# Optimization experiments

Hardware: AMD Instinct MI355X
Metric: run time of the kernel (lower is better)

Reference implementation:

```python
import jax, jax.numpy as jnp
import numpy as np

DIM = 512
HEADS = 8
BLOCKS = 6
DFF = 2048
B = 4
T = 2048
VOCAB = 20
CLASSES = 1
MAX_TOKENS = 5000
EPS = 1e-5


def _make_pe():
    # Sinusoidal positional encoding, identical to PositionalEncodingSin
    pos = np.arange(MAX_TOKENS, dtype=np.float32)[:, None]
    div = np.exp(np.arange(0, DIM, 2, dtype=np.float32) * (-np.log(10000.0) / DIM))
    pe = np.zeros((MAX_TOKENS, DIM), dtype=np.float32)
    pe[:, 0::2] = np.sin(pos * div)
    pe[:, 1::2] = np.cos(pos * div)
    return jnp.asarray(pe)


def setup_inputs() -> dict:
    key = jax.random.key(0)
    ks = jax.random.split(key, 8)

    def n(k, shape, s=0.02):
        return (jax.random.normal(k, shape) * s).astype(jnp.float32)

    x = jax.random.randint(ks[0], (B, T), 0, VOCAB, dtype=jnp.int32)
    embed = n(ks[1], (VOCAB, DIM))
    pe = _make_pe()
    Wqkv = n(ks[2], (BLOCKS, DIM, 3 * DIM))   # to_qvk (no bias)
    W0 = n(ks[3], (BLOCKS, DIM, DIM))          # W_0 (no bias)
    g1 = jnp.ones((BLOCKS, DIM), jnp.float32)
    b1 = jnp.zeros((BLOCKS, DIM), jnp.float32)
    g2 = jnp.ones((BLOCKS, DIM), jnp.float32)
    b2 = jnp.zeros((BLOCKS, DIM), jnp.float32)
    Wl1 = n(ks[4], (BLOCKS, DIM, DFF))
    bl1 = jnp.zeros((BLOCKS, DFF), jnp.float32)
    Wl2 = n(ks[5], (BLOCKS, DFF, DIM))
    bl2 = jnp.zeros((BLOCKS, DIM), jnp.float32)
    Whead = n(ks[6], (DIM, CLASSES))
    bhead = jnp.zeros((CLASSES,), jnp.float32)
    return dict(x=x, embed=embed, pe=pe, Wqkv=Wqkv, W0=W0, g1=g1, b1=b1,
                g2=g2, b2=b2, Wl1=Wl1, bl1=bl1, Wl2=Wl2, bl2=bl2,
                Whead=Whead, bhead=bhead)


def _ln(x, g, b):
    mu = x.mean(-1, keepdims=True)
    var = ((x - mu) ** 2).mean(-1, keepdims=True)
    return (x - mu) / jnp.sqrt(var + EPS) * g + b


def _mhsa(x, Wqkv, W0):
    b, t, _ = x.shape
    dh = DIM // HEADS
    qkv = x @ Wqkv                                   # [b, t, 3*DIM]
    # rearrange 'b t (d k h) -> k b h t d' with k=3, h=HEADS
    qkv = qkv.reshape(b, t, dh, 3, HEADS).transpose(3, 0, 4, 1, 2)
    q, k, v = qkv[0], qkv[1], qkv[2]                 # [b, h, t, dh]
    scores = jnp.einsum('bhid,bhjd->bhij', q, k) * (dh ** -0.5)
    attn = jax.nn.softmax(scores, axis=-1)
    out = jnp.einsum('bhij,bhjd->bhid', attn, v)
    out = out.transpose(0, 2, 1, 3).reshape(b, t, DIM)  # 'b h t d -> b t (h d)'
    return out @ W0


def _forward(x, embed, pe, Wqkv, W0, g1, b1, g2, b2, Wl1, bl1, Wl2, bl2, Whead, bhead):
    h = embed[x] + pe[None, :x.shape[1], :]          # embedding + sinusoidal PE (dropout off)
    for i in range(BLOCKS):                          # post-norm transformer blocks
        a = _mhsa(h, Wqkv[i], W0[i])
        y = _ln(a + h, g1[i], b1[i])
        m = jax.nn.gelu(y @ Wl1[i] + bl1[i], approximate=False) @ Wl2[i] + bl2[i]
        h = _ln(m + y, g2[i], b2[i])
    return (h @ Whead + bhead).squeeze(-1)           # [B, T]


def reference(x, embed, pe, Wqkv, W0, g1, b1, g2, b2, Wl1, bl1, Wl2, bl2, Whead, bhead):
    return _forward(x, embed, pe, Wqkv, W0, g1, b1, g2, b2, Wl1, bl1, Wl2, bl2, Whead, bhead)
```

## Files before the change

kernel.cpp:

```cpp
#include <hip/hip_runtime.h>
#include <hip/hip_bf16.h>
#include <math.h>

#define DIMD 512
#define HEADS 8
#define NBLK 6
#define DFF 2048
#define BATCH 4
#define SEQ 2048
#define NTOK 8192
#define DH 64
#define LNEPS 1e-5f
#define QSCALE 0.1803368801111204f

typedef __bf16 bf16;
typedef __bf16 bf16x8 __attribute__((ext_vector_type(8)));
typedef __bf16 bf16x4 __attribute__((ext_vector_type(4)));
typedef float f32x4 __attribute__((ext_vector_type(4)));
typedef float f32x16 __attribute__((ext_vector_type(16)));

__device__ __forceinline__ void async16(const void* g, void* l) {
  __builtin_amdgcn_global_load_lds(
      (const __attribute__((address_space(1))) void*)g,
      (__attribute__((address_space(3))) void*)l, 16, 0, 0);
}

__device__ __forceinline__ int swz(int r) { return ((r >> 1) ^ (r >> 3)) & 3; }

__global__ void k_cvt_t(const float* __restrict__ in, bf16* __restrict__ out, int K, int N) {
  __shared__ float T[32][33];
  const float* src = in + (size_t)blockIdx.z * K * N;
  bf16* dst = out + (size_t)blockIdx.z * K * N;
  int k0 = blockIdx.y * 32, n0 = blockIdx.x * 32;
  int r = threadIdx.x >> 3, c4 = (threadIdx.x & 7) * 4;
  float4 v = *reinterpret_cast<const float4*>(src + (size_t)(k0 + r) * N + n0 + c4);
  T[r][c4] = v.x; T[r][c4 + 1] = v.y; T[r][c4 + 2] = v.z; T[r][c4 + 3] = v.w;
  __syncthreads();
  bf16x4 o;
  o[0] = (bf16)T[c4][r]; o[1] = (bf16)T[c4 + 1][r];
  o[2] = (bf16)T[c4 + 2][r]; o[3] = (bf16)T[c4 + 3][r];
  *reinterpret_cast<bf16x4*>(dst + (size_t)(n0 + r) * K + k0 + c4) = o;
}

__global__ void k_cvt_qkv(const float* __restrict__ in, bf16* __restrict__ out, int K, int N) {
  __shared__ float T[32][33];
  const float* src = in + (size_t)blockIdx.z * K * N;
  bf16* dst = out + (size_t)blockIdx.z * K * N;
  int k0 = blockIdx.y * 32, n0 = blockIdx.x * 32;
  int r = threadIdx.x >> 3, c4 = (threadIdx.x & 7) * 4;
  float4 v = *reinterpret_cast<const float4*>(src + (size_t)(k0 + r) * N + n0 + c4);
  T[r][c4] = v.x; T[r][c4 + 1] = v.y; T[r][c4 + 2] = v.z; T[r][c4 + 3] = v.w;
  __syncthreads();
  int n_src = n0 + r;
  int d = n_src / 24;
  int rem = n_src - d * 24;
  int np = (rem >> 3) * 512 + (rem & 7) * 64 + d;
  bf16x4 o;
  o[0] = (bf16)T[c4][r]; o[1] = (bf16)T[c4 + 1][r];
  o[2] = (bf16)T[c4 + 2][r]; o[3] = (bf16)T[c4 + 3][r];
  *reinterpret_cast<bf16x4*>(dst + (size_t)np * K + k0 + c4) = o;
}

__global__ void k_embed(const int* __restrict__ x, const float* __restrict__ embed,
                        const float* __restrict__ pe, bf16* __restrict__ hb,
                        float* __restrict__ hf) {
  int row = blockIdx.x;
  int t = row & (SEQ - 1);
  int tok = x[row];
  int c = threadIdx.x * 2;
  const float* e = embed + (size_t)tok * DIMD;
  const float* p = pe + (size_t)t * DIMD;
  float v0 = e[c] + p[c];
  float v1 = e[c + 1] + p[c + 1];
  size_t o = (size_t)row * DIMD + c;
  hb[o] = (bf16)v0; hb[o + 1] = (bf16)v1;
  hf[o] = v0;       hf[o + 1] = v1;
}

enum { EPI_QKV = 0, EPI_RES = 1, EPI_GELU = 2, EPI_BIASRES = 3 };

template <int EPI, int MT>
__global__ __launch_bounds__(256) void k_gemm(
    const bf16* __restrict__ A, const bf16* __restrict__ Wt,
    const float* __restrict__ bias, const float* __restrict__ resf,
    bf16* __restrict__ out0, bf16* __restrict__ out1, bf16* __restrict__ out2,
    float* __restrict__ outf, int N, int K) {
  constexpr int TJ = (MT == 128) ? 2 : 1;
  __shared__ bf16 As[2][MT][32];
  __shared__ bf16 Bs[2][128][32];
  int tid = threadIdx.x;
  int w = tid >> 6, lane = tid & 63, hi = lane >> 5, l31 = lane & 31;
  int m0 = blockIdx.y * MT, n0 = blockIdx.x * 128;
  int wr = (MT == 128) ? (w >> 1) : 0;
  int wc = (MT == 128) ? (w & 1) : w;

  const bf16 *Ag0, *Ag1 = nullptr, *Bg0, *Bg1;
  int dA0, dA1 = 0, dB0, dB1;
  if (MT == 128) {
    int ra0 = w * 32 + (lane >> 2), ra1 = ra0 + 16;
    Ag0 = A + (size_t)(m0 + ra0) * K + ((lane & 3) ^ swz(ra0)) * 8;
    Ag1 = A + (size_t)(m0 + ra1) * K + ((lane & 3) ^ swz(ra1)) * 8;
    Bg0 = Wt + (size_t)(n0 + ra0) * K + ((lane & 3) ^ swz(ra0)) * 8;
    Bg1 = Wt + (size_t)(n0 + ra1) * K + ((lane & 3) ^ swz(ra1)) * 8;
    dA0 = w * 1024; dA1 = dA0 + 512;
    dB0 = w * 1024; dB1 = dB0 + 512;
  } else {
    int ra = w * 16 + (lane >> 2);
    Ag0 = A + (size_t)(m0 + ra) * K + ((lane & 3) ^ swz(ra)) * 8;
    int rb1 = ra + 64;
    Bg0 = Wt + (size_t)(n0 + ra) * K + ((lane & 3) ^ swz(ra)) * 8;
    Bg1 = Wt + (size_t)(n0 + rb1) * K + ((lane & 3) ^ swz(rb1)) * 8;
    dA0 = w * 512;
    dB0 = w * 512; dB1 = dB0 + 2048;
  }

  int rowA[2], fA[2], colB[2], fB[2];
#pragma unroll
  for (int i = 0; i < 2; ++i) {
    rowA[i] = ((MT == 128) ? wr * 64 : 0) + i * 32 + l31;
    fA[i] = swz(rowA[i]);
  }
#pragma unroll
  for (int j = 0; j < TJ; ++j) {
    colB[j] = ((MT == 128) ? (wc * 64 + j * 32) : (wc * 32)) + l31;
    fB[j] = swz(colB[j]);
  }

  f32x16 acc[2][TJ] = {};

  auto stage = [&](int it) {
    int buf = it & 1;
    bf16* a = &As[buf][0][0];
    bf16* b = &Bs[buf][0][0];
    int k0 = it * 32;
    async16(Ag0 + k0, a + dA0);
    if (MT == 128) async16(Ag1 + k0, a + dA1);
    async16(Bg0 + k0, b + dB0);
    async16(Bg1 + k0, b + dB1);
  };

  int nit = K / 32;
  stage(0);
  for (int it = 0; it < nit; ++it) {
    int buf = it & 1;
    __syncthreads();
    if (it + 1 < nit) stage(it + 1);
#pragma unroll
    for (int s = 0; s < 2; ++s) {
      int lc = s * 2 + hi;
      bf16x8 af[2], bfr[TJ];
#pragma unroll
      for (int i = 0; i < 2; ++i)
        af[i] = *reinterpret_cast<const bf16x8*>(&As[buf][rowA[i]][(lc ^ fA[i]) * 8]);
#pragma unroll
      for (int j = 0; j < TJ; ++j)
        bfr[j] = *reinterpret_cast<const bf16x8*>(&Bs[buf][colB[j]][(lc ^ fB[j]) * 8]);
#pragma unroll
      for (int i = 0; i < 2; ++i)
#pragma unroll
        for (int j = 0; j < TJ; ++j)
          acc[i][j] = __builtin_amdgcn_mfma_f32_32x32x16_bf16(af[i], bfr[j], acc[i][j], 0, 0, 0);
    }
  }

#pragma unroll
  for (int j = 0; j < TJ; ++j) {
    int col = n0 + ((MT == 128) ? (wc * 64 + j * 32) : (wc * 32)) + l31;
    int qwhich = 0, qhh = 0, qdd = 0;
    float bcol = 0.f;
    if (EPI == EPI_QKV) {
      qwhich = col >> 9; qhh = (col >> 6) & 7; qdd = col & 63;
    } else if (EPI == EPI_GELU || EPI == EPI_BIASRES) {
      bcol = bias[col];
    }
#pragma unroll
    for (int i = 0; i < 2; ++i) {
#pragma unroll
      for (int reg = 0; reg < 16; ++reg) {
        int row = m0 + ((MT == 128) ? wr * 64 : 0) + i * 32 + (reg & 3) + 8 * (reg >> 2) + 4 * hi;
        float v = acc[i][j][reg];
        if (EPI == EPI_QKV) {
          int b = row >> 11;
          int t = row & (SEQ - 1);
          int bh = b * HEADS + qhh;
          if (qwhich == 0)      out0[((size_t)bh * SEQ + t) * DH + qdd] = (bf16)(v * QSCALE);
          else if (qwhich == 1) out1[((size_t)bh * SEQ + t) * DH + qdd] = (bf16)v;
          else                  out2[((size_t)bh * DH + qdd) * SEQ + t] = (bf16)v;
        } else if (EPI == EPI_RES) {
          outf[(size_t)row * N + col] = v + resf[(size_t)row * N + col];
        } else if (EPI == EPI_GELU) {
          float xv = v + bcol;
          out0[(size_t)row * N + col] = (bf16)(0.5f * xv * (1.0f + erff(xv * 0.70710678118f)));
        } else {
          outf[(size_t)row * N + col] = v + bcol + resf[(size_t)row * N + col];
        }
      }
    }
  }
}

__global__ __launch_bounds__(256) void k_attn(const bf16* __restrict__ q,
                                              const bf16* __restrict__ k,
                                              const bf16* __restrict__ vt,
                                              bf16* __restrict__ out) {
  __shared__ bf16 Ks[64][64];
  __shared__ bf16 Vs[64][64];
  __shared__ bf16 Pw[4][2][16][72];
  int tid = threadIdx.x;
  int w = tid >> 6, lane = tid & 63, quad = lane >> 4, l15 = lane & 15;
  int f = blockIdx.y * gridDim.x + blockIdx.x;
  int xcd = f & 7, g = f >> 3;
  int bh = xcd * 4 + (g >> 4);
  int qt = g & 15;
  const bf16* qbase = q + (size_t)bh * SEQ * DH;
  const bf16* kbase = k + (size_t)bh * SEQ * DH;
  const bf16* vbase = vt + (size_t)bh * DH * SEQ;

  bf16x8 qf[2][2];
#pragma unroll
  for (int s = 0; s < 2; ++s) {
    int qrow = qt * 128 + s * 64 + w * 16 + l15;
    qf[s][0] = *reinterpret_cast<const bf16x8*>(qbase + (size_t)qrow * DH + quad * 8);
    qf[s][1] = *reinterpret_cast<const bf16x8*>(qbase + (size_t)qrow * DH + 32 + quad * 8);
  }

  int strow = w * 16 + (lane >> 3);
  int scol = ((lane & 7) ^ (lane >> 3)) * 8;
  const bf16* kp = kbase + (size_t)strow * DH + scol;
  const bf16* vp = vbase + (size_t)strow * SEQ + scol;
  bf16* kdst = &Ks[0][0] + (size_t)w * 1024 + (size_t)lane * 8;
  bf16* vdst = &Vs[0][0] + (size_t)w * 1024 + (size_t)lane * 8;

  f32x4 Ot[2][4] = {};
  float ls[2] = {0.f, 0.f};
  int fx = (l15 & 7);

  bf16x8 ka0 = *reinterpret_cast<const bf16x8*>(kp);
  bf16x8 kb0 = *reinterpret_cast<const bf16x8*>(kp + (size_t)8 * DH);
  bf16x8 va0 = *reinterpret_cast<const bf16x8*>(vp);
  bf16x8 vb0 = *reinterpret_cast<const bf16x8*>(vp + (size_t)8 * SEQ);
  bf16x8 ka1 = *reinterpret_cast<const bf16x8*>(kp + (size_t)64 * DH);
  bf16x8 kb1 = *reinterpret_cast<const bf16x8*>(kp + (size_t)72 * DH);
  bf16x8 va1 = *reinterpret_cast<const bf16x8*>(vp + 64);
  bf16x8 vb1 = *reinterpret_cast<const bf16x8*>(vp + 64 + (size_t)8 * SEQ);

  const int nit = SEQ / 64;
  auto body = [&](int it, bf16x8& ka, bf16x8& kb, bf16x8& va, bf16x8& vb) {
    __syncthreads();
    *reinterpret_cast<bf16x8*>(kdst) = ka;
    *reinterpret_cast<bf16x8*>(kdst + 512) = kb;
    *reinterpret_cast<bf16x8*>(vdst) = va;
    *reinterpret_cast<bf16x8*>(vdst + 512) = vb;
    __syncthreads();
    if (it + 2 < nit) {
      size_t ko = (size_t)(it + 2) * 64;
      ka = *reinterpret_cast<const bf16x8*>(kp + ko * DH);
      kb = *reinterpret_cast<const bf16x8*>(kp + ko * DH + 8 * DH);
      va = *reinterpret_cast<const bf16x8*>(vp + ko);
      vb = *reinterpret_cast<const bf16x8*>(vp + ko + (size_t)8 * SEQ);
    }

    f32x4 st[2][4];
#pragma unroll
    for (int nt = 0; nt < 4; ++nt) {
      bf16x8 kf0 = *reinterpret_cast<const bf16x8*>(&Ks[nt * 16 + l15][(quad ^ fx) * 8]);
      bf16x8 kf1 = *reinterpret_cast<const bf16x8*>(&Ks[nt * 16 + l15][((quad + 4) ^ fx) * 8]);
#pragma unroll
      for (int s = 0; s < 2; ++s) {
        f32x4 z = {};
        z = __builtin_amdgcn_mfma_f32_16x16x32_bf16(kf0, qf[s][0], z, 0, 0, 0);
        z = __builtin_amdgcn_mfma_f32_16x16x32_bf16(kf1, qf[s][1], z, 0, 0, 0);
        st[s][nt] = z;
      }
    }

#pragma unroll
    for (int s = 0; s < 2; ++s)
#pragma unroll
      for (int nt = 0; nt < 4; ++nt) {
#pragma unroll
        for (int r = 0; r < 4; ++r) {
          float p = exp2f(st[s][nt][r]);
          st[s][nt][r] = p;
          ls[s] += p;
        }
        bf16x4 pv;
        pv[0] = (bf16)st[s][nt][0]; pv[1] = (bf16)st[s][nt][1];
        pv[2] = (bf16)st[s][nt][2]; pv[3] = (bf16)st[s][nt][3];
        *reinterpret_cast<bf16x4*>(&Pw[w][s][l15][nt * 16 + quad * 4]) = pv;
      }

#pragma unroll
    for (int h = 0; h < 2; ++h) {
      bf16x8 pf0 = *reinterpret_cast<const bf16x8*>(&Pw[w][0][l15][h * 32 + quad * 8]);
      bf16x8 pf1 = *reinterpret_cast<const bf16x8*>(&Pw[w][1][l15][h * 32 + quad * 8]);
#pragma unroll
      for (int nt = 0; nt < 4; ++nt) {
        bf16x8 vf = *reinterpret_cast<const bf16x8*>(&Vs[nt * 16 + l15][((quad + 4 * h) ^ fx) * 8]);
        Ot[0][nt] = __builtin_amdgcn_mfma_f32_16x16x32_bf16(vf, pf0, Ot[0][nt], 0, 0, 0);
        Ot[1][nt] = __builtin_amdgcn_mfma_f32_16x16x32_bf16(vf, pf1, Ot[1][nt], 0, 0, 0);
      }
    }
  };

  for (int it = 0; it < nit; it += 2) {
    body(it, ka0, kb0, va0, vb0);
    body(it + 1, ka1, kb1, va1, vb1);
  }

  int b = bh >> 3, hh = bh & 7;
  int qr = lane >> 2, c0 = (lane & 3) * 16;
#pragma unroll
  for (int s = 0; s < 2; ++s) {
    float l = ls[s];
    l += __shfl_xor(l, 16);
    l += __shfl_xor(l, 32);
    float inv = 1.0f / l;
#pragma unroll
    for (int nt = 0; nt < 4; ++nt) {
      bf16x4 ov;
      ov[0] = (bf16)(Ot[s][nt][0] * inv); ov[1] = (bf16)(Ot[s][nt][1] * inv);
      ov[2] = (bf16)(Ot[s][nt][2] * inv); ov[3] = (bf16)(Ot[s][nt][3] * inv);
      *reinterpret_cast<bf16x4*>(&Pw[w][s][l15][nt * 16 + quad * 4]) = ov;
    }
    bf16x8 o0 = *reinterpret_cast<const bf16x8*>(&Pw[w][s][qr][c0]);
    bf16x8 o1 = *reinterpret_cast<const bf16x8*>(&Pw[w][s][qr][c0 + 8]);
    int token = b * SEQ + qt * 128 + s * 64 + w * 16 + qr;
    *reinterpret_cast<bf16x8*>(out + (size_t)token * DIMD + hh * DH + c0) = o0;
    *reinterpret_cast<bf16x8*>(out + (size_t)token * DIMD + hh * DH + c0 + 8) = o1;
  }
}

__global__ void k_ln(const float* __restrict__ in, const float* __restrict__ g,
                     const float* __restrict__ b, bf16* __restrict__ outb,
                     float* __restrict__ outf) {
  int wid = (blockIdx.x * blockDim.x + threadIdx.x) >> 6;
  int lane = threadIdx.x & 63;
  const float* row = in + (size_t)wid * DIMD;
  float4 x0 = *reinterpret_cast<const float4*>(row + lane * 8);
  float4 x1 = *reinterpret_cast<const float4*>(row + lane * 8 + 4);
  float xs[8] = {x0.x, x0.y, x0.z, x0.w, x1.x, x1.y, x1.z, x1.w};
  float s = 0.f, sq = 0.f;
#pragma unroll
  for (int j = 0; j < 8; ++j) { s += xs[j]; sq += xs[j] * xs[j]; }
#pragma unroll
  for (int m = 1; m < 64; m <<= 1) { s += __shfl_xor(s, m); sq += __shfl_xor(sq, m); }
  float mu = s * (1.0f / DIMD);
  float var = sq * (1.0f / DIMD) - mu * mu;
  float rstd = rsqrtf(var + LNEPS);
  bf16x8 ov;
#pragma unroll
  for (int j = 0; j < 8; ++j) {
    int c = lane * 8 + j;
    float y = (xs[j] - mu) * rstd * g[c] + b[c];
    ov[j] = (bf16)y;
    outf[(size_t)wid * DIMD + c] = y;
  }
  *reinterpret_cast<bf16x8*>(outb + (size_t)wid * DIMD + lane * 8) = ov;
}

__global__ void k_head(const bf16* __restrict__ h, const float* __restrict__ w,
                       const float* __restrict__ bh, float* __restrict__ out) {
  int row = (blockIdx.x * blockDim.x + threadIdx.x) >> 6;
  int lane = threadIdx.x & 63;
  bf16x8 xv = *reinterpret_cast<const bf16x8*>(h + (size_t)row * DIMD + lane * 8);
  float s = 0.f;
#pragma unroll
  for (int j = 0; j < 8; ++j) s += (float)xv[j] * w[lane * 8 + j];
#pragma unroll
  for (int m = 1; m < 64; m <<= 1) s += __shfl_xor(s, m);
  if (lane == 0) out[row] = s + bh[0];
}

extern "C" void kernel_launch(void* const* d_in, const int* in_sizes, int n_in,
                              void* d_out, int out_size, void* d_ws, size_t ws_size,
                              hipStream_t stream) {
  const int*   x     = (const int*)d_in[0];
  const float* embed = (const float*)d_in[1];
  const float* pe    = (const float*)d_in[2];
  const float* Wqkv  = (const float*)d_in[3];
  const float* W0    = (const float*)d_in[4];
  const float* g1    = (const float*)d_in[5];
  const float* b1    = (const float*)d_in[6];
  const float* g2    = (const float*)d_in[7];
  const float* b2    = (const float*)d_in[8];
  const float* Wl1   = (const float*)d_in[9];
  const float* bl1   = (const float*)d_in[10];
  const float* Wl2   = (const float*)d_in[11];
  const float* bl2   = (const float*)d_in[12];
  const float* Whead = (const float*)d_in[13];
  const float* bhead = (const float*)d_in[14];
  float* outp = (float*)d_out;

  char* ws = (char*)d_ws;
  size_t off = 0;
  auto alloc = [&](size_t bytes) { void* p = ws + off; off += (bytes + 255) & ~(size_t)255; return p; };
  const size_t ACT = (size_t)NTOK * DIMD;
  bf16*  hb   = (bf16*)alloc(ACT * 2);
  float* hf   = (float*)alloc(ACT * 4);
  bf16*  qb   = (bf16*)alloc(ACT * 2);
  bf16*  kb   = (bf16*)alloc(ACT * 2);
  bf16*  vtb  = (bf16*)alloc(ACT * 2);
  bf16*  ao   = (bf16*)alloc(ACT * 2);
  float* r32  = (float*)alloc(ACT * 4);
  bf16*  yb   = (bf16*)alloc(ACT * 2);
  float* yf   = (float*)alloc(ACT * 4);
  bf16*  wqkt = (bf16*)alloc((size_t)NBLK * DIMD * 3 * DIMD * 2);
  bf16*  w0t  = (bf16*)alloc((size_t)NBLK * DIMD * DIMD * 2);
  bf16*  wl1t = (bf16*)alloc((size_t)NBLK * DIMD * DFF * 2);
  bf16*  wl2t = (bf16*)alloc((size_t)NBLK * DFF * DIMD * 2);
  bf16*  mid  = qb;

  k_cvt_qkv<<<dim3(3 * DIMD / 32, DIMD / 32, NBLK), 256, 0, stream>>>(Wqkv, wqkt, DIMD, 3 * DIMD);
  k_cvt_t<<<dim3(DIMD / 32, DIMD / 32, NBLK), 256, 0, stream>>>(W0, w0t, DIMD, DIMD);
  k_cvt_t<<<dim3(DFF / 32, DIMD / 32, NBLK), 256, 0, stream>>>(Wl1, wl1t, DIMD, DFF);
  k_cvt_t<<<dim3(DIMD / 32, DFF / 32, NBLK), 256, 0, stream>>>(Wl2, wl2t, DFF, DIMD);

  k_embed<<<NTOK, 256, 0, stream>>>(x, embed, pe, hb, hf);
  for (int i = 0; i < NBLK; ++i) {
    k_gemm<EPI_QKV, 128><<<dim3(3 * DIMD / 128, NTOK / 128), 256, 0, stream>>>(
        hb, wqkt + (size_t)i * DIMD * 3 * DIMD, nullptr, nullptr,
        qb, kb, vtb, nullptr, 3 * DIMD, DIMD);
    k_attn<<<dim3(SEQ / 128, BATCH * HEADS), 256, 0, stream>>>(qb, kb, vtb, ao);
    k_gemm<EPI_RES, 64><<<dim3(DIMD / 128, NTOK / 64), 256, 0, stream>>>(
        ao, w0t + (size_t)i * DIMD * DIMD, nullptr, hf,
        nullptr, nullptr, nullptr, r32, DIMD, DIMD);
    k_ln<<<NTOK / 4, 256, 0, stream>>>(r32, g1 + i * DIMD, b1 + i * DIMD, yb, yf);
    k_gemm<EPI_GELU, 128><<<dim3(DFF / 128, NTOK / 128), 256, 0, stream>>>(
        yb, wl1t + (size_t)i * DIMD * DFF, bl1 + (size_t)i * DFF, nullptr,
        mid, nullptr, nullptr, nullptr, DFF, DIMD);
    k_gemm<EPI_BIASRES, 64><<<dim3(DIMD / 128, NTOK / 64), 256, 0, stream>>>(
        mid, wl2t + (size_t)i * DFF * DIMD, bl2 + (size_t)i * DIMD, yf,
        nullptr, nullptr, nullptr, r32, DIMD, DFF);
    k_ln<<<NTOK / 4, 256, 0, stream>>>(r32, g2 + i * DIMD, b2 + i * DIMD, hb, hf);
  }
  k_head<<<NTOK / 4, 256, 0, stream>>>(hb, Whead, bhead, outp);
}
```

Before: 1.443 ms.

## Keep residual stream in bf16 and drop GEMM LDS double buffering

The fp32 residual and pre-LayerNorm buffers are removed. GEMM epilogues now read a bf16 residual and write a bf16 pre-norm sum, and LayerNorm reads bf16 and writes only bf16, which roughly halves residual traffic and removes the extra fp32 writes. The GEMM main loop also changes from a double-buffered async-load pipeline to a single buffer with loads followed by two barriers per k-step. That gives up load/compute overlap for less LDS, and carrying the residual in bf16 lowers numerical accuracy across six blocks.

```diff
diff --git a/kernel.cpp b/kernel.cpp
--- a/kernel.cpp
+++ b/kernel.cpp
@@ -62,19 +62,16 @@
 }
 
 __global__ void k_embed(const int* __restrict__ x, const float* __restrict__ embed,
-                        const float* __restrict__ pe, bf16* __restrict__ hb,
-                        float* __restrict__ hf) {
+                        const float* __restrict__ pe, bf16* __restrict__ hb) {
   int row = blockIdx.x;
   int t = row & (SEQ - 1);
   int tok = x[row];
   int c = threadIdx.x * 2;
   const float* e = embed + (size_t)tok * DIMD;
   const float* p = pe + (size_t)t * DIMD;
-  float v0 = e[c] + p[c];
-  float v1 = e[c + 1] + p[c + 1];
   size_t o = (size_t)row * DIMD + c;
-  hb[o] = (bf16)v0; hb[o + 1] = (bf16)v1;
-  hf[o] = v0;       hf[o + 1] = v1;
+  hb[o] = (bf16)(e[c] + p[c]);
+  hb[o + 1] = (bf16)(e[c + 1] + p[c + 1]);
 }
 
 enum { EPI_QKV = 0, EPI_RES = 1, EPI_GELU = 2, EPI_BIASRES = 3 };
@@ -82,12 +79,12 @@
 template <int EPI, int MT>
 __global__ __launch_bounds__(256) void k_gemm(
     const bf16* __restrict__ A, const bf16* __restrict__ Wt,
-    const float* __restrict__ bias, const float* __restrict__ resf,
+    const float* __restrict__ bias, const bf16* __restrict__ resb,
     bf16* __restrict__ out0, bf16* __restrict__ out1, bf16* __restrict__ out2,
-    float* __restrict__ outf, int N, int K) {
+    int N, int K) {
   constexpr int TJ = (MT == 128) ? 2 : 1;
-  __shared__ bf16 As[2][MT][32];
-  __shared__ bf16 Bs[2][128][32];
+  __shared__ bf16 As[MT][32];
+  __shared__ bf16 Bs[128][32];
   int tid = threadIdx.x;
   int w = tid >> 6, lane = tid & 63, hi = lane >> 5, l31 = lane & 31;
   int m0 = blockIdx.y * MT, n0 = blockIdx.x * 128;
@@ -95,23 +92,23 @@
   int wc = (MT == 128) ? (w & 1) : w;
 
   const bf16 *Ag0, *Ag1 = nullptr, *Bg0, *Bg1;
-  int dA0, dA1 = 0, dB0, dB1;
+  bf16 *dA0, *dA1 = nullptr, *dB0, *dB1;
   if (MT == 128) {
     int ra0 = w * 32 + (lane >> 2), ra1 = ra0 + 16;
     Ag0 = A + (size_t)(m0 + ra0) * K + ((lane & 3) ^ swz(ra0)) * 8;
     Ag1 = A + (size_t)(m0 + ra1) * K + ((lane & 3) ^ swz(ra1)) * 8;
     Bg0 = Wt + (size_t)(n0 + ra0) * K + ((lane & 3) ^ swz(ra0)) * 8;
     Bg1 = Wt + (size_t)(n0 + ra1) * K + ((lane & 3) ^ swz(ra1)) * 8;
-    dA0 = w * 1024; dA1 = dA0 + 512;
-    dB0 = w * 1024; dB1 = dB0 + 512;
+    dA0 = &As[0][0] + w * 1024; dA1 = dA0 + 512;
+    dB0 = &Bs[0][0] + w * 1024; dB1 = dB0 + 512;
   } else {
     int ra = w * 16 + (lane >> 2);
     Ag0 = A + (size_t)(m0 + ra) * K + ((lane & 3) ^ swz(ra)) * 8;
     int rb1 = ra + 64;
     Bg0 = Wt + (size_t)(n0 + ra) * K + ((lane & 3) ^ swz(ra)) * 8;
     Bg1 = Wt + (size_t)(n0 + rb1) * K + ((lane & 3) ^ swz(rb1)) * 8;
-    dA0 = w * 512;
-    dB0 = w * 512; dB1 = dB0 + 2048;
+    dA0 = &As[0][0] + w * 512;
+    dB0 = &Bs[0][0] + w * 512; dB1 = dB0 + 2048;
   }
 
   int rowA[2], fA[2], colB[2], fB[2];
@@ -128,39 +125,30 @@
 
   f32x16 acc[2][TJ] = {};
 
-  auto stage = [&](int it) {
-    int buf = it & 1;
-    bf16* a = &As[buf][0][0];
-    bf16* b = &Bs[buf][0][0];
-    int k0 = it * 32;
-    async16(Ag0 + k0, a + dA0);
-    if (MT == 128) async16(Ag1 + k0, a + dA1);
-    async16(Bg0 + k0, b + dB0);
-    async16(Bg1 + k0, b + dB1);
-  };
-
-  int nit = K / 32;
-  stage(0);
-  for (int it = 0; it < nit; ++it) {
-    int buf = it & 1;
+  for (int k0 = 0; k0 < K; k0 += 32) {
+    async16(Ag0 + k0, dA0);
+    if (MT == 128) async16(Ag1 + k0, dA1);
+    async16(Bg0 + k0, dB0);
+    async16(Bg1 + k0, dB1);
     __syncthreads();
-    if (it + 1 < nit) stage(it + 1);
+
 #pragma unroll
     for (int s = 0; s < 2; ++s) {
       int lc = s * 2 + hi;
       bf16x8 af[2], bfr[TJ];
 #pragma unroll
       for (int i = 0; i < 2; ++i)
-        af[i] = *reinterpret_cast<const bf16x8*>(&As[buf][rowA[i]][(lc ^ fA[i]) * 8]);
+        af[i] = *reinterpret_cast<const bf16x8*>(&As[rowA[i]][(lc ^ fA[i]) * 8]);
 #pragma unroll
       for (int j = 0; j < TJ; ++j)
-        bfr[j] = *reinterpret_cast<const bf16x8*>(&Bs[buf][colB[j]][(lc ^ fB[j]) * 8]);
+        bfr[j] = *reinterpret_cast<const bf16x8*>(&Bs[colB[j]][(lc ^ fB[j]) * 8]);
 #pragma unroll
       for (int i = 0; i < 2; ++i)
 #pragma unroll
         for (int j = 0; j < TJ; ++j)
           acc[i][j] = __builtin_amdgcn_mfma_f32_32x32x16_bf16(af[i], bfr[j], acc[i][j], 0, 0, 0);
     }
+    __syncthreads();
   }
 
 #pragma unroll
@@ -187,12 +175,12 @@
           else if (qwhich == 1) out1[((size_t)bh * SEQ + t) * DH + qdd] = (bf16)v;
           else                  out2[((size_t)bh * DH + qdd) * SEQ + t] = (bf16)v;
         } else if (EPI == EPI_RES) {
-          outf[(size_t)row * N + col] = v + resf[(size_t)row * N + col];
+          out0[(size_t)row * N + col] = (bf16)(v + (float)resb[(size_t)row * N + col]);
         } else if (EPI == EPI_GELU) {
           float xv = v + bcol;
           out0[(size_t)row * N + col] = (bf16)(0.5f * xv * (1.0f + erff(xv * 0.70710678118f)));
         } else {
-          outf[(size_t)row * N + col] = v + bcol + resf[(size_t)row * N + col];
+          out0[(size_t)row * N + col] = (bf16)(v + bcol + (float)resb[(size_t)row * N + col]);
         }
       }
     }
@@ -331,18 +319,15 @@
   }
 }
 
-__global__ void k_ln(const float* __restrict__ in, const float* __restrict__ g,
-                     const float* __restrict__ b, bf16* __restrict__ outb,
-                     float* __restrict__ outf) {
+__global__ void k_ln(const bf16* __restrict__ in, const float* __restrict__ g,
+                     const float* __restrict__ b, bf16* __restrict__ outb) {
   int wid = (blockIdx.x * blockDim.x + threadIdx.x) >> 6;
   int lane = threadIdx.x & 63;
-  const float* row = in + (size_t)wid * DIMD;
-  float4 x0 = *reinterpret_cast<const float4*>(row + lane * 8);
-  float4 x1 = *reinterpret_cast<const float4*>(row + lane * 8 + 4);
-  float xs[8] = {x0.x, x0.y, x0.z, x0.w, x1.x, x1.y, x1.z, x1.w};
+  bf16x8 xv = *reinterpret_cast<const bf16x8*>(in + (size_t)wid * DIMD + lane * 8);
+  float xs[8];
   float s = 0.f, sq = 0.f;
 #pragma unroll
-  for (int j = 0; j < 8; ++j) { s += xs[j]; sq += xs[j] * xs[j]; }
+  for (int j = 0; j < 8; ++j) { xs[j] = (float)xv[j]; s += xs[j]; sq += xs[j] * xs[j]; }
 #pragma unroll
   for (int m = 1; m < 64; m <<= 1) { s += __shfl_xor(s, m); sq += __shfl_xor(sq, m); }
   float mu = s * (1.0f / DIMD);
@@ -352,9 +337,7 @@
 #pragma unroll
   for (int j = 0; j < 8; ++j) {
     int c = lane * 8 + j;
-    float y = (xs[j] - mu) * rstd * g[c] + b[c];
-    ov[j] = (bf16)y;
-    outf[(size_t)wid * DIMD + c] = y;
+    ov[j] = (bf16)((xs[j] - mu) * rstd * g[c] + b[c]);
   }
   *reinterpret_cast<bf16x8*>(outb + (size_t)wid * DIMD + lane * 8) = ov;
 }
@@ -397,14 +380,12 @@
   auto alloc = [&](size_t bytes) { void* p = ws + off; off += (bytes + 255) & ~(size_t)255; return p; };
   const size_t ACT = (size_t)NTOK * DIMD;
   bf16*  hb   = (bf16*)alloc(ACT * 2);
-  float* hf   = (float*)alloc(ACT * 4);
   bf16*  qb   = (bf16*)alloc(ACT * 2);
   bf16*  kb   = (bf16*)alloc(ACT * 2);
   bf16*  vtb  = (bf16*)alloc(ACT * 2);
   bf16*  ao   = (bf16*)alloc(ACT * 2);
-  float* r32  = (float*)alloc(ACT * 4);
+  bf16*  rb   = (bf16*)alloc(ACT * 2);
   bf16*  yb   = (bf16*)alloc(ACT * 2);
-  float* yf   = (float*)alloc(ACT * 4);
   bf16*  wqkt = (bf16*)alloc((size_t)NBLK * DIMD * 3 * DIMD * 2);
   bf16*  w0t  = (bf16*)alloc((size_t)NBLK * DIMD * DIMD * 2);
   bf16*  wl1t = (bf16*)alloc((size_t)NBLK * DIMD * DFF * 2);
@@ -416,23 +397,23 @@
   k_cvt_t<<<dim3(DFF / 32, DIMD / 32, NBLK), 256, 0, stream>>>(Wl1, wl1t, DIMD, DFF);
   k_cvt_t<<<dim3(DIMD / 32, DFF / 32, NBLK), 256, 0, stream>>>(Wl2, wl2t, DFF, DIMD);
 
-  k_embed<<<NTOK, 256, 0, stream>>>(x, embed, pe, hb, hf);
+  k_embed<<<NTOK, 256, 0, stream>>>(x, embed, pe, hb);
   for (int i = 0; i < NBLK; ++i) {
     k_gemm<EPI_QKV, 128><<<dim3(3 * DIMD / 128, NTOK / 128), 256, 0, stream>>>(
         hb, wqkt + (size_t)i * DIMD * 3 * DIMD, nullptr, nullptr,
-        qb, kb, vtb, nullptr, 3 * DIMD, DIMD);
+        qb, kb, vtb, 3 * DIMD, DIMD);
     k_attn<<<dim3(SEQ / 128, BATCH * HEADS), 256, 0, stream>>>(qb, kb, vtb, ao);
     k_gemm<EPI_RES, 64><<<dim3(DIMD / 128, NTOK / 64), 256, 0, stream>>>(
-        ao, w0t + (size_t)i * DIMD * DIMD, nullptr, hf,
-        nullptr, nullptr, nullptr, r32, DIMD, DIMD);
-    k_ln<<<NTOK / 4, 256, 0, stream>>>(r32, g1 + i * DIMD, b1 + i * DIMD, yb, yf);
+        ao, w0t + (size_t)i * DIMD * DIMD, nullptr, hb,
+        rb, nullptr, nullptr, DIMD, DIMD);
+    k_ln<<<NTOK / 4, 256, 0, stream>>>(rb, g1 + i * DIMD, b1 + i * DIMD, yb);
     k_gemm<EPI_GELU, 128><<<dim3(DFF / 128, NTOK / 128), 256, 0, stream>>>(
         yb, wl1t + (size_t)i * DIMD * DFF, bl1 + (size_t)i * DFF, nullptr,
-        mid, nullptr, nullptr, nullptr, DFF, DIMD);
+        mid, nullptr, nullptr, DFF, DIMD);
     k_gemm<EPI_BIASRES, 64><<<dim3(DIMD / 128, NTOK / 64), 256, 0, stream>>>(
-        mid, wl2t + (size_t)i * DFF * DIMD, bl2 + (size_t)i * DIMD, yf,
-        nullptr, nullptr, nullptr, r32, DIMD, DFF);
-    k_ln<<<NTOK / 4, 256, 0, stream>>>(r32, g2 + i * DIMD, b2 + i * DIMD, hb, hf);
+        mid, wl2t + (size_t)i * DFF * DIMD, bl2 + (size_t)i * DIMD, yb,
+        rb, nullptr, nullptr, DIMD, DFF);
+    k_ln<<<NTOK / 4, 256, 0, stream>>>(rb, g2 + i * DIMD, b2 + i * DIMD, hb);
   }
   k_head<<<NTOK / 4, 256, 0, stream>>>(hb, Whead, bhead, outp);
 }
```

Result: faster. 1.319 ms (-8.6%).
